# Kernel tuning notes

Hardware: AMD Instinct MI355X
Metric: run time of the kernel (lower is better)

## Reference

```python
import jax, jax.numpy as jnp
import numpy as np

B, S, D, H = 2, 2048, 1024, 16
DH = D // H  # dim_per_head = 64


def setup_inputs() -> dict:
    key = jax.random.key(0)
    ks = jax.random.split(key, 12)
    scale = 1.0 / np.sqrt(D)
    inp = {
        "key": jax.random.normal(ks[0], (B, S, D), jnp.float32),
        "value": jax.random.normal(ks[1], (B, S, D), jnp.float32),
        "query": jax.random.normal(ks[2], (B, S, D), jnp.float32),
        "mask": jax.random.randint(ks[3], (B, S, S), 0, 2) == 1,
        "Wq": jax.random.normal(ks[4], (D, D), jnp.float32) * scale,
        "bq": jnp.zeros((D,), jnp.float32),
        "Wk": jax.random.normal(ks[5], (D, D), jnp.float32) * scale,
        "bk": jnp.zeros((D,), jnp.float32),
        "Wv": jax.random.normal(ks[6], (D, D), jnp.float32) * scale,
        "bv": jnp.zeros((D,), jnp.float32),
        "Wo": jax.random.normal(ks[7], (D, D), jnp.float32) * scale,
        "bo": jnp.zeros((D,), jnp.float32),
    }
    return inp


def reference(key, value, query, mask, Wq, bq, Wk, bk, Wv, bv, Wo, bo):
    b, s, d = query.shape
    dh = d // H

    def split_heads(x):  # [b, s, d] -> [b, H, s, dh]
        return x.reshape(b, -1, H, dh).transpose(0, 2, 1, 3)

    q = split_heads(query @ Wq + bq) / jnp.sqrt(jnp.float32(dh))
    k = split_heads(key @ Wk + bk)
    v = split_heads(value @ Wv + bv)

    scores = jnp.einsum("bhqd,bhkd->bhqk", q, k)  # [b, H, s, s]
    scores = jnp.where(mask[:, None, :, :], jnp.float32(-1e18), scores)
    attn = jax.nn.softmax(scores, axis=-1)  # dropout is identity in eval
    ctx = jnp.einsum("bhqk,bhkd->bhqd", attn, v)
    ctx = ctx.transpose(0, 2, 1, 3).reshape(b, s, d)
    return ctx @ Wo + bo
```

## Files before the change

kernel.cpp:

```cpp
#include <hip/hip_runtime.h>
#include <hip/hip_bf16.h>

#define BATCH  2
#define SEQ    2048
#define DMODEL 1024
#define NHEAD  16
#define DHEAD  64
#define NTOK   (BATCH * SEQ)

using f32x4  = __attribute__((ext_vector_type(4))) float;
using f32x16 = __attribute__((ext_vector_type(16))) float;
using s16x4  = __attribute__((ext_vector_type(4))) short;
using s16x8  = __attribute__((ext_vector_type(8))) short;

__device__ __forceinline__ short f2bf(float f) {
  __hip_bfloat16 h = __float2bfloat16(f);
  return *(short*)&h;
}

__device__ __forceinline__ void gload_lds16(const short* g, short* l) {
  __builtin_amdgcn_global_load_lds(
      (const __attribute__((address_space(1))) void*)g,
      (__attribute__((address_space(3))) void*)l, 16, 0, 0);
}

__global__ __launch_bounds__(256) void wtrans_kernel(
    const float* __restrict__ Wq, const float* __restrict__ Wk,
    const float* __restrict__ Wv, const float* __restrict__ Wo,
    short* __restrict__ Wt) {
  __shared__ short tile[64][72];
  const float* W = blockIdx.z == 0 ? Wq : blockIdx.z == 1 ? Wk
                 : blockIdx.z == 2 ? Wv : Wo;
  short* out = Wt + (size_t)blockIdx.z * DMODEL * DMODEL;
  int k0 = blockIdx.x * 64, n0 = blockIdx.y * 64;
  int t = threadIdx.x;
#pragma unroll
  for (int i = 0; i < 4; ++i) {
    int idx = t + i * 256;
    int row = idx >> 4, c4 = idx & 15;
    f32x4 v = *(const f32x4*)(W + (size_t)(k0 + row) * DMODEL + n0 + c4 * 4);
    s16x4 p;
    p[0] = f2bf(v[0]); p[1] = f2bf(v[1]); p[2] = f2bf(v[2]); p[3] = f2bf(v[3]);
    *(s16x4*)&tile[row][c4 * 4] = p;
  }
  __syncthreads();
#pragma unroll
  for (int i = 0; i < 2; ++i) {
    int idx = t + i * 256;
    int nrow = idx >> 3, c8 = idx & 7;
    s16x8 p;
#pragma unroll
    for (int j = 0; j < 8; ++j) p[j] = tile[c8 * 8 + j][nrow];
    *(s16x8*)(out + (size_t)(n0 + nrow) * DMODEL + k0 + c8 * 8) = p;
  }
}

__global__ __launch_bounds__(256) void xcast_kernel(
    const float* __restrict__ Xq, const float* __restrict__ Xk,
    const float* __restrict__ Xv, short* __restrict__ Xb) {
  int sel = blockIdx.y;
  const float* src = sel == 0 ? Xq : sel == 1 ? Xk : Xv;
  size_t off = ((size_t)blockIdx.x * 256 + threadIdx.x) * 8;
  f32x4 v0 = *(const f32x4*)(src + off);
  f32x4 v1 = *(const f32x4*)(src + off + 4);
  s16x8 p;
  p[0] = f2bf(v0[0]); p[1] = f2bf(v0[1]); p[2] = f2bf(v0[2]); p[3] = f2bf(v0[3]);
  p[4] = f2bf(v1[0]); p[5] = f2bf(v1[1]); p[6] = f2bf(v1[2]); p[7] = f2bf(v1[3]);
  *(s16x8*)(Xb + (size_t)sel * NTOK * DMODEL + off) = p;
}

__global__ __launch_bounds__(256) void mpack_kernel(
    const int* __restrict__ mask, unsigned long long* __restrict__ Mp) {
  const int total_words = BATCH * SEQ * (SEQ / 64);
  int lane = threadIdx.x & 63;
  int wv = blockIdx.x * 4 + (threadIdx.x >> 6);
  int nw = gridDim.x * 4;
  for (int w = wv; w < total_words; w += nw) {
    int mv = mask[(size_t)w * 64 + lane];
    unsigned long long bits = __ballot(mv != 0);
    if (lane == 0) Mp[w] = bits;
  }
}

__global__ __launch_bounds__(256) void proj_qkv_kernel(
    const short* __restrict__ Xb, const short* __restrict__ Wt,
    const float* __restrict__ bq, const float* __restrict__ bk,
    const float* __restrict__ bv, short* __restrict__ QKV) {
  __shared__ short As[2][128 * 32];
  __shared__ short Bs[2][128 * 32];
  int wg = blockIdx.x;
  int orig = (wg & 7) * 96 + (wg >> 3);
  int sel = orig >> 8;
  int rem = orig & 255;
  int mx = rem >> 3, ny = rem & 7;

  const short* X    = Xb + (size_t)sel * NTOK * DMODEL;
  const float* bias = sel == 0 ? bq : sel == 1 ? bk : bv;
  const short* Wsel = Wt + (size_t)sel * DMODEL * DMODEL;
  short* Obuf = QKV + (size_t)sel * ((size_t)BATCH * NHEAD * SEQ * DHEAD);
  const float scale = sel == 0 ? 0.18033688011111793f : 1.0f;

  int m0 = mx * 128, n0 = ny * 128;
  int t = threadIdx.x, wid = t >> 6, lane = t & 63;
  int lr = lane & 15, lg = lane >> 4;
  int wr = wid >> 1, wc = wid & 1;
  f32x4 acc[4][4] = {};

  const int gr0 = t >> 2, gc0 = (t & 3) << 3;
  const short* Ax0 = X + (size_t)(m0 + gr0) * DMODEL + gc0;
  const short* Ax1 = Ax0 + (size_t)64 * DMODEL;
  const short* Bw0 = Wsel + (size_t)(n0 + gr0) * DMODEL + gc0;
  const short* Bw1 = Bw0 + (size_t)64 * DMODEL;
  const int lofs0 = (t & ~63) << 3, lofs1 = lofs0 + 256 * 8;

#define STAGEQ(bufi, k0s) {                                                   \
    gload_lds16(Ax0 + (k0s), &As[bufi][0] + lofs0);                           \
    gload_lds16(Ax1 + (k0s), &As[bufi][0] + lofs1);                           \
    gload_lds16(Bw0 + (k0s), &Bs[bufi][0] + lofs0);                           \
    gload_lds16(Bw1 + (k0s), &Bs[bufi][0] + lofs1); }

  STAGEQ(0, 0);
  __syncthreads();

  int cur = 0;
  for (int kt = 0; kt < DMODEL / 32; ++kt) {
    if (kt + 1 < DMODEL / 32) STAGEQ(cur ^ 1, (kt + 1) * 32);
    s16x8 afr[4], bfr[4];
#pragma unroll
    for (int mi = 0; mi < 4; ++mi)
      afr[mi] = *(const s16x8*)(&As[cur][0] + (wr * 64 + mi * 16 + lr) * 32 + lg * 8);
#pragma unroll
    for (int ni = 0; ni < 4; ++ni)
      bfr[ni] = *(const s16x8*)(&Bs[cur][0] + (wc * 64 + ni * 16 + lr) * 32 + lg * 8);
    __builtin_amdgcn_s_setprio(1);
#pragma unroll
    for (int mi = 0; mi < 4; ++mi)
#pragma unroll
      for (int ni = 0; ni < 4; ++ni)
        acc[mi][ni] = __builtin_amdgcn_mfma_f32_16x16x32_bf16(
            afr[mi], bfr[ni], acc[mi][ni], 0, 0, 0);
    __builtin_amdgcn_s_setprio(0);
    __syncthreads();
    cur ^= 1;
  }
#undef STAGEQ

  if (sel == 2) {
    int bq_ = m0 >> 11;
    int s0 = (m0 & (SEQ - 1)) + wr * 64 + lg * 4;
#pragma unroll
    for (int mi = 0; mi < 4; ++mi)
#pragma unroll
      for (int ni = 0; ni < 4; ++ni) {
        int n = n0 + wc * 64 + ni * 16 + lr;
        float bv_ = bias[n];
        int h = n >> 6, d = n & 63;
        s16x4 pk;
#pragma unroll
        for (int r = 0; r < 4; ++r) pk[r] = f2bf(acc[mi][ni][r] + bv_);
        *(s16x4*)&Obuf[((size_t)(bq_ * NHEAD + h) * DHEAD + d) * SEQ
                       + s0 + mi * 16] = pk;
      }
  } else {
#pragma unroll
    for (int mi = 0; mi < 4; ++mi)
#pragma unroll
      for (int ni = 0; ni < 4; ++ni) {
        int n = n0 + wc * 64 + ni * 16 + lr;
        float bv_ = bias[n];
        int h = n >> 6, d = n & 63;
#pragma unroll
        for (int r = 0; r < 4; ++r) {
          int m = m0 + wr * 64 + mi * 16 + lg * 4 + r;
          int b = m >> 11, s = m & (SEQ - 1);
          float val = (acc[mi][ni][r] + bv_) * scale;
          Obuf[((size_t)(b * NHEAD + h) * SEQ + s) * DHEAD + d] = f2bf(val);
        }
      }
  }
}

__global__ __launch_bounds__(256) void attn_kernel(
    const short* __restrict__ Qb, const short* __restrict__ Kb,
    const short* __restrict__ VbT, const unsigned long long* __restrict__ Mp,
    short* __restrict__ Ctx) {
  __shared__ short Ks[2][64 * 64];
  __shared__ short Vt[2][64 * 64];
  int wg = blockIdx.x;
  int orig = (wg & 7) * 64 + (wg >> 3);
  int bh = orig >> 4, qt = orig & 15;
  int b = bh >> 4, h = bh & 15;
  int q0 = qt * 128;
  int t = threadIdx.x, wid = t >> 6, lane = t & 63;
  int ql = lane & 31, hi = lane >> 5;
  int qrow = q0 + wid * 32 + ql;

  const short* Qp = Qb + ((size_t)bh * SEQ + qrow) * DHEAD + hi * 8;
  s16x8 qf[4];
#pragma unroll
  for (int ds = 0; ds < 4; ++ds) qf[ds] = *(const s16x8*)(Qp + ds * 16);

  const short* KbB = Kb + (size_t)bh * SEQ * DHEAD;
  const short* VtB = VbT + (size_t)bh * DHEAD * SEQ;

  const int srow = lane >> 3;
  const int schunk = ((lane & 7) ^ srow) * 8;

  int offK[4];
#pragma unroll
  for (int j = 0; j < 4; ++j)
    offK[j] = ql * 64 + (((j * 2 + hi) ^ (ql & 7)) << 3);
  int offVa[4], offVb[4];
#pragma unroll
  for (int m = 0; m < 4; ++m) {
    offVa[m] = ql * 64 + (((m * 2)     ^ (ql & 7)) << 3) + 4 * hi;
    offVb[m] = ql * 64 + (((m * 2 + 1) ^ (ql & 7)) << 3) + 4 * hi;
  }

  float m_run = -1e30f, l_run = 0.f;
  f32x16 oacc0 = {}, oacc1 = {};

  const unsigned long long* mrow = Mp + ((size_t)b * SEQ + qrow) * (SEQ / 64);

#define STAGE(bufi, k0s)                                                      \
  {                                                                           \
    _Pragma("unroll")                                                         \
    for (int i = 0; i < 2; ++i) {                                             \
      int rbase = wid * 16 + i * 8;                                           \
      gload_lds16(KbB + (size_t)((k0s) + rbase + srow) * DHEAD + schunk,      \
                  &Ks[bufi][rbase * 64]);                                     \
      gload_lds16(VtB + (size_t)(rbase + srow) * SEQ + (k0s) + schunk,        \
                  &Vt[bufi][rbase * 64]);                                     \
    }                                                                         \
  }

  unsigned long long mw_cur = mrow[0];
  STAGE(0, 0);
  asm volatile("s_waitcnt vmcnt(0)" ::: "memory");
  __syncthreads();

  int cur = 0;
  for (int kt = 0; kt < SEQ / 64; ++kt) {
    unsigned long long mw_next = 0;
    if (kt + 1 < SEQ / 64) {
      STAGE(cur ^ 1, (kt + 1) * 64);
      mw_next = mrow[kt + 1];
    }
    const short* KsC = Ks[cur];
    const short* VtC = Vt[cur];

    f32x16 sf0 = {}, sf1 = {};
    __builtin_amdgcn_s_setprio(1);
#pragma unroll
    for (int ds = 0; ds < 4; ++ds) {
      s16x8 k0 = *(const s16x8*)&KsC[offK[ds]];
      s16x8 k1 = *(const s16x8*)&KsC[offK[ds] + 2048];
      sf0 = __builtin_amdgcn_mfma_f32_32x32x16_bf16(k0, qf[ds], sf0, 0, 0, 0);
      sf1 = __builtin_amdgcn_mfma_f32_32x32x16_bf16(k1, qf[ds], sf1, 0, 0, 0);
    }
    __builtin_amdgcn_s_setprio(0);

    unsigned h0 = ((unsigned)mw_cur) >> (hi << 2);
    unsigned h1 = ((unsigned)(mw_cur >> 32)) >> (hi << 2);
#pragma unroll
    for (int r = 0; r < 16; ++r) {
      const int c = (r & 3) + 8 * (r >> 2);
      if ((h0 >> c) & 1u) sf0[r] = -1e30f;
      if ((h1 >> c) & 1u) sf1[r] = -1e30f;
    }

    float tm = sf0[0];
#pragma unroll
    for (int r = 1; r < 16; ++r) tm = fmaxf(tm, sf0[r]);
#pragma unroll
    for (int r = 0; r < 16; ++r) tm = fmaxf(tm, sf1[r]);
    tm = fmaxf(tm, __shfl_xor(tm, 32, 64));

    bool small = __all(tm <= m_run + 8.0f);
    if (!small) {
      float mnew = fmaxf(m_run, tm);
      float scl = __builtin_amdgcn_exp2f(m_run - mnew);
      m_run = mnew;
      l_run *= scl;
#pragma unroll
      for (int r = 0; r < 16; ++r) {
        float s_ = __shfl(scl, (r & 3) + 8 * (r >> 2) + 4 * hi, 64);
        oacc0[r] *= s_;
        oacc1[r] *= s_;
      }
    }

    float ss = 0.f;
#pragma unroll
    for (int r = 0; r < 16; ++r) {
      sf0[r] = __builtin_amdgcn_exp2f(sf0[r] - m_run);
      sf1[r] = __builtin_amdgcn_exp2f(sf1[r] - m_run);
      ss += sf0[r] + sf1[r];
    }
    l_run += ss + __shfl_xor(ss, 32, 64);

    __builtin_amdgcn_s_setprio(1);
#pragma unroll
    for (int m = 0; m < 4; ++m) {
      const int base = (m & 1) * 8;
      s16x8 pa;
#pragma unroll
      for (int e = 0; e < 8; ++e)
        pa[e] = f2bf(m < 2 ? sf0[base + e] : sf1[base + e]);
      union { s16x4 q[2]; s16x8 v; } v0, v1;
      v0.q[0] = *(const s16x4*)&VtC[offVa[m]];
      v0.q[1] = *(const s16x4*)&VtC[offVb[m]];
      v1.q[0] = *(const s16x4*)&VtC[offVa[m] + 2048];
      v1.q[1] = *(const s16x4*)&VtC[offVb[m] + 2048];
      oacc0 = __builtin_amdgcn_mfma_f32_32x32x16_bf16(pa, v0.v, oacc0, 0, 0, 0);
      oacc1 = __builtin_amdgcn_mfma_f32_32x32x16_bf16(pa, v1.v, oacc1, 0, 0, 0);
    }
    __builtin_amdgcn_s_setprio(0);

    asm volatile("s_waitcnt vmcnt(0)" ::: "memory");
    __syncthreads();
    cur ^= 1;
    mw_cur = mw_next;
  }
#undef STAGE

#pragma unroll
  for (int r = 0; r < 16; ++r) {
    int c = (r & 3) + 8 * (r >> 2) + 4 * hi;
    float linv = 1.0f / __shfl(l_run, c, 64);
    int q_ = q0 + wid * 32 + c;
    size_t base = ((size_t)b * SEQ + q_) * DMODEL + h * DHEAD + ql;
    Ctx[base] = f2bf(oacc0[r] * linv);
    Ctx[base + 32] = f2bf(oacc1[r] * linv);
  }
}

__global__ __launch_bounds__(256) void proj_out_kernel(
    const short* __restrict__ Ctx, const short* __restrict__ Wot,
    const float* __restrict__ bo, float* __restrict__ Out) {
  __shared__ short As[2][128 * 32];
  __shared__ short Bs[2][128 * 32];
  int wg = blockIdx.x;
  int orig = (wg & 7) * 32 + (wg >> 3);
  int mx = orig >> 3, ny = orig & 7;
  int m0 = mx * 128, n0 = ny * 128;
  int t = threadIdx.x, wid = t >> 6, lane = t & 63;
  int lr = lane & 15, lg = lane >> 4;
  int wr = wid >> 1, wc = wid & 1;
  f32x4 acc[4][4] = {};

  const int gr0 = t >> 2, gc0 = (t & 3) << 3;
  const short* Actx0 = Ctx + (size_t)(m0 + gr0) * DMODEL + gc0;
  const short* Actx1 = Actx0 + (size_t)64 * DMODEL;
  const short* Bwo0 = Wot + (size_t)(n0 + gr0) * DMODEL + gc0;
  const short* Bwo1 = Bwo0 + (size_t)64 * DMODEL;
  const int lofs0 = (t & ~63) << 3, lofs1 = lofs0 + 256 * 8;

#define STAGE_PO(bufi, k0s) {                                                 \
    gload_lds16(Actx0 + (k0s), &As[bufi][0] + lofs0);                         \
    gload_lds16(Actx1 + (k0s), &As[bufi][0] + lofs1);                         \
    gload_lds16(Bwo0 + (k0s), &Bs[bufi][0] + lofs0);                          \
    gload_lds16(Bwo1 + (k0s), &Bs[bufi][0] + lofs1); }

  STAGE_PO(0, 0);
  __syncthreads();

  int cur = 0;
  for (int kt = 0; kt < DMODEL / 32; ++kt) {
    if (kt + 1 < DMODEL / 32) STAGE_PO(cur ^ 1, (kt + 1) * 32);
    s16x8 afr[4], bfr[4];
#pragma unroll
    for (int mi = 0; mi < 4; ++mi)
      afr[mi] = *(const s16x8*)(&As[cur][0] + (wr * 64 + mi * 16 + lr) * 32 + lg * 8);
#pragma unroll
    for (int ni = 0; ni < 4; ++ni)
      bfr[ni] = *(const s16x8*)(&Bs[cur][0] + (wc * 64 + ni * 16 + lr) * 32 + lg * 8);
    __builtin_amdgcn_s_setprio(1);
#pragma unroll
    for (int mi = 0; mi < 4; ++mi)
#pragma unroll
      for (int ni = 0; ni < 4; ++ni)
        acc[mi][ni] = __builtin_amdgcn_mfma_f32_16x16x32_bf16(
            afr[mi], bfr[ni], acc[mi][ni], 0, 0, 0);
    __builtin_amdgcn_s_setprio(0);
    __syncthreads();
    cur ^= 1;
  }
#undef STAGE_PO

#pragma unroll
  for (int mi = 0; mi < 4; ++mi)
#pragma unroll
    for (int ni = 0; ni < 4; ++ni) {
      int n = n0 + wc * 64 + ni * 16 + lr;
      float bv_ = bo[n];
#pragma unroll
      for (int r = 0; r < 4; ++r) {
        int m = m0 + wr * 64 + mi * 16 + lg * 4 + r;
        Out[(size_t)m * DMODEL + n] = acc[mi][ni][r] + bv_;
      }
    }
}

extern "C" void kernel_launch(void* const* d_in, const int* in_sizes, int n_in,
                              void* d_out, int out_size, void* d_ws, size_t ws_size,
                              hipStream_t stream) {
  const float* key_in   = (const float*)d_in[0];
  const float* value_in = (const float*)d_in[1];
  const float* query_in = (const float*)d_in[2];
  const int*   mask     = (const int*)d_in[3];
  const float* Wq = (const float*)d_in[4];
  const float* bq = (const float*)d_in[5];
  const float* Wk = (const float*)d_in[6];
  const float* bk = (const float*)d_in[7];
  const float* Wv = (const float*)d_in[8];
  const float* bv = (const float*)d_in[9];
  const float* Wo = (const float*)d_in[10];
  const float* bo = (const float*)d_in[11];
  float* out = (float*)d_out;

  short* ws = (short*)d_ws;
  const size_t WSZ   = (size_t)DMODEL * DMODEL;
  const size_t QKVSZ = (size_t)BATCH * NHEAD * SEQ * DHEAD;
  short* Wt  = ws;
  short* QKV = ws + 4 * WSZ;
  short* Qb  = QKV;
  short* Kb  = QKV + QKVSZ;
  short* VbT = QKV + 2 * QKVSZ;
  short* Xb  = ws + 4 * WSZ + 3 * QKVSZ;
  short* Ctx = Xb;
  unsigned long long* Mp = (unsigned long long*)ws;

  wtrans_kernel<<<dim3(16, 16, 4), 256, 0, stream>>>(Wq, Wk, Wv, Wo, Wt);
  xcast_kernel<<<dim3(2048, 3), 256, 0, stream>>>(query_in, key_in, value_in, Xb);
  proj_qkv_kernel<<<dim3(768), 256, 0, stream>>>(Xb, Wt, bq, bk, bv, QKV);
  mpack_kernel<<<dim3(1024), 256, 0, stream>>>(mask, Mp);
  attn_kernel<<<dim3(512), 256, 0, stream>>>(Qb, Kb, VbT, Mp, Ctx);
  proj_out_kernel<<<dim3(256), 256, 0, stream>>>(Ctx, Wt + 3 * WSZ, bo, out);
}
```

Measured before the change: 183.9 us.

## Merge prep kernels and triple-buffer LDS pipelines in GEMMs and attention

Fuses the weight transpose, input cast and mask packing into one prep kernel and moves the packed mask buffer into the output buffer, so the mask packing no longer has to wait for the QKV projection. Switches the QKV projection, attention and output projection loops from double to triple-buffered LDS staging, using partial vmcnt waits and one barrier per iteration to hide load latency. In attention it also defers the cross-half max and sum shuffles, doing the sum once at the end. Raises LDS use per block, which may lower occupancy, and relies on the output buffer being overwritten only after attention has read the mask.

```diff
diff --git a/kernel.cpp b/kernel.cpp
--- a/kernel.cpp
+++ b/kernel.cpp
@@ -24,61 +24,58 @@
       (__attribute__((address_space(3))) void*)l, 16, 0, 0);
 }
 
-__global__ __launch_bounds__(256) void wtrans_kernel(
+__global__ __launch_bounds__(256) void prep_kernel(
     const float* __restrict__ Wq, const float* __restrict__ Wk,
     const float* __restrict__ Wv, const float* __restrict__ Wo,
-    short* __restrict__ Wt) {
+    short* __restrict__ Wt,
+    const float* __restrict__ Xq, const float* __restrict__ Xk,
+    const float* __restrict__ Xv, short* __restrict__ Xb,
+    const int* __restrict__ mask, unsigned long long* __restrict__ Mp) {
   __shared__ short tile[64][72];
-  const float* W = blockIdx.z == 0 ? Wq : blockIdx.z == 1 ? Wk
-                 : blockIdx.z == 2 ? Wv : Wo;
-  short* out = Wt + (size_t)blockIdx.z * DMODEL * DMODEL;
-  int k0 = blockIdx.x * 64, n0 = blockIdx.y * 64;
-  int t = threadIdx.x;
-#pragma unroll
-  for (int i = 0; i < 4; ++i) {
-    int idx = t + i * 256;
-    int row = idx >> 4, c4 = idx & 15;
-    f32x4 v = *(const f32x4*)(W + (size_t)(k0 + row) * DMODEL + n0 + c4 * 4);
-    s16x4 p;
-    p[0] = f2bf(v[0]); p[1] = f2bf(v[1]); p[2] = f2bf(v[2]); p[3] = f2bf(v[3]);
-    *(s16x4*)&tile[row][c4 * 4] = p;
-  }
-  __syncthreads();
-#pragma unroll
-  for (int i = 0; i < 2; ++i) {
-    int idx = t + i * 256;
-    int nrow = idx >> 3, c8 = idx & 7;
+  int bid = blockIdx.x, t = threadIdx.x;
+  if (bid < 1024) {
+    int z = bid >> 8, rem = bid & 255, x = rem & 15, y = rem >> 4;
+    const float* W = z == 0 ? Wq : z == 1 ? Wk : z == 2 ? Wv : Wo;
+    short* out = Wt + (size_t)z * DMODEL * DMODEL;
+    int k0 = x * 64, n0 = y * 64;
+#pragma unroll
+    for (int i = 0; i < 4; ++i) {
+      int idx = t + i * 256, row = idx >> 4, c4 = idx & 15;
+      f32x4 v = *(const f32x4*)(W + (size_t)(k0 + row) * DMODEL + n0 + c4 * 4);
+      s16x4 p;
+      p[0] = f2bf(v[0]); p[1] = f2bf(v[1]); p[2] = f2bf(v[2]); p[3] = f2bf(v[3]);
+      *(s16x4*)&tile[row][c4 * 4] = p;
+    }
+    __syncthreads();
+#pragma unroll
+    for (int i = 0; i < 2; ++i) {
+      int idx = t + i * 256, nrow = idx >> 3, c8 = idx & 7;
+      s16x8 p;
+#pragma unroll
+      for (int j = 0; j < 8; ++j) p[j] = tile[c8 * 8 + j][nrow];
+      *(s16x8*)(out + (size_t)(n0 + nrow) * DMODEL + k0 + c8 * 8) = p;
+    }
+  } else if (bid < 7168) {
+    int r = bid - 1024;
+    int sel = r >> 11, bx = r & 2047;
+    const float* src = sel == 0 ? Xq : sel == 1 ? Xk : Xv;
+    size_t off = ((size_t)bx * 256 + t) * 8;
+    f32x4 v0 = *(const f32x4*)(src + off);
+    f32x4 v1 = *(const f32x4*)(src + off + 4);
     s16x8 p;
-#pragma unroll
-    for (int j = 0; j < 8; ++j) p[j] = tile[c8 * 8 + j][nrow];
-    *(s16x8*)(out + (size_t)(n0 + nrow) * DMODEL + k0 + c8 * 8) = p;
-  }
-}
-
-__global__ __launch_bounds__(256) void xcast_kernel(
-    const float* __restrict__ Xq, const float* __restrict__ Xk,
-    const float* __restrict__ Xv, short* __restrict__ Xb) {
-  int sel = blockIdx.y;
-  const float* src = sel == 0 ? Xq : sel == 1 ? Xk : Xv;
-  size_t off = ((size_t)blockIdx.x * 256 + threadIdx.x) * 8;
-  f32x4 v0 = *(const f32x4*)(src + off);
-  f32x4 v1 = *(const f32x4*)(src + off + 4);
-  s16x8 p;
-  p[0] = f2bf(v0[0]); p[1] = f2bf(v0[1]); p[2] = f2bf(v0[2]); p[3] = f2bf(v0[3]);
-  p[4] = f2bf(v1[0]); p[5] = f2bf(v1[1]); p[6] = f2bf(v1[2]); p[7] = f2bf(v1[3]);
-  *(s16x8*)(Xb + (size_t)sel * NTOK * DMODEL + off) = p;
-}
-
-__global__ __launch_bounds__(256) void mpack_kernel(
-    const int* __restrict__ mask, unsigned long long* __restrict__ Mp) {
-  const int total_words = BATCH * SEQ * (SEQ / 64);
-  int lane = threadIdx.x & 63;
-  int wv = blockIdx.x * 4 + (threadIdx.x >> 6);
-  int nw = gridDim.x * 4;
-  for (int w = wv; w < total_words; w += nw) {
-    int mv = mask[(size_t)w * 64 + lane];
-    unsigned long long bits = __ballot(mv != 0);
-    if (lane == 0) Mp[w] = bits;
+    p[0] = f2bf(v0[0]); p[1] = f2bf(v0[1]); p[2] = f2bf(v0[2]); p[3] = f2bf(v0[3]);
+    p[4] = f2bf(v1[0]); p[5] = f2bf(v1[1]); p[6] = f2bf(v1[2]); p[7] = f2bf(v1[3]);
+    *(s16x8*)(Xb + (size_t)sel * NTOK * DMODEL + off) = p;
+  } else {
+    int bx = bid - 7168;
+    const int total_words = BATCH * SEQ * (SEQ / 64);
+    int lane = t & 63;
+    int wv = bx * 4 + (t >> 6);
+    for (int w = wv; w < total_words; w += 4096) {
+      int mv = mask[(size_t)w * 64 + lane];
+      unsigned long long bits = __ballot(mv != 0);
+      if (lane == 0) Mp[w] = bits;
+    }
   }
 }
 
@@ -86,8 +83,8 @@
     const short* __restrict__ Xb, const short* __restrict__ Wt,
     const float* __restrict__ bq, const float* __restrict__ bk,
     const float* __restrict__ bv, short* __restrict__ QKV) {
-  __shared__ short As[2][128 * 32];
-  __shared__ short Bs[2][128 * 32];
+  __shared__ short As[3][128 * 32];
+  __shared__ short Bs[3][128 * 32];
   int wg = blockIdx.x;
   int orig = (wg & 7) * 96 + (wg >> 3);
   int sel = orig >> 8;
@@ -120,18 +117,25 @@
     gload_lds16(Bw1 + (k0s), &Bs[bufi][0] + lofs1); }
 
   STAGEQ(0, 0);
-  __syncthreads();
-
-  int cur = 0;
-  for (int kt = 0; kt < DMODEL / 32; ++kt) {
-    if (kt + 1 < DMODEL / 32) STAGEQ(cur ^ 1, (kt + 1) * 32);
+  STAGEQ(1, 32);
+
+  int cb = 0;
+  for (int kt = 0; kt < 32; ++kt) {
+    if (kt + 1 < 32) { asm volatile("s_waitcnt vmcnt(4)" ::: "memory"); }
+    else             { asm volatile("s_waitcnt vmcnt(0)" ::: "memory"); }
+    __builtin_amdgcn_sched_barrier(0);
+    __builtin_amdgcn_s_barrier();
+    __builtin_amdgcn_sched_barrier(0);
+    int st = cb + 2; if (st > 2) st -= 3;
+    if (kt + 2 < 32) STAGEQ(st, (kt + 2) * 32);
+
     s16x8 afr[4], bfr[4];
 #pragma unroll
     for (int mi = 0; mi < 4; ++mi)
-      afr[mi] = *(const s16x8*)(&As[cur][0] + (wr * 64 + mi * 16 + lr) * 32 + lg * 8);
+      afr[mi] = *(const s16x8*)(&As[cb][0] + (wr * 64 + mi * 16 + lr) * 32 + lg * 8);
 #pragma unroll
     for (int ni = 0; ni < 4; ++ni)
-      bfr[ni] = *(const s16x8*)(&Bs[cur][0] + (wc * 64 + ni * 16 + lr) * 32 + lg * 8);
+      bfr[ni] = *(const s16x8*)(&Bs[cb][0] + (wc * 64 + ni * 16 + lr) * 32 + lg * 8);
     __builtin_amdgcn_s_setprio(1);
 #pragma unroll
     for (int mi = 0; mi < 4; ++mi)
@@ -140,8 +144,7 @@
         acc[mi][ni] = __builtin_amdgcn_mfma_f32_16x16x32_bf16(
             afr[mi], bfr[ni], acc[mi][ni], 0, 0, 0);
     __builtin_amdgcn_s_setprio(0);
-    __syncthreads();
-    cur ^= 1;
+    cb = (cb == 2) ? 0 : cb + 1;
   }
 #undef STAGEQ
 
@@ -184,8 +187,8 @@
     const short* __restrict__ Qb, const short* __restrict__ Kb,
     const short* __restrict__ VbT, const unsigned long long* __restrict__ Mp,
     short* __restrict__ Ctx) {
-  __shared__ short Ks[2][64 * 64];
-  __shared__ short Vt[2][64 * 64];
+  __shared__ short Ks[3][64 * 64];
+  __shared__ short Vt[3][64 * 64];
   int wg = blockIdx.x;
   int orig = (wg & 7) * 64 + (wg >> 3);
   int bh = orig >> 4, qt = orig & 15;
@@ -234,20 +237,25 @@
     }                                                                         \
   }
 
-  unsigned long long mw_cur = mrow[0];
+  unsigned long long mwq0 = mrow[0], mwq1 = mrow[1];
   STAGE(0, 0);
-  asm volatile("s_waitcnt vmcnt(0)" ::: "memory");
-  __syncthreads();
-
-  int cur = 0;
-  for (int kt = 0; kt < SEQ / 64; ++kt) {
-    unsigned long long mw_next = 0;
-    if (kt + 1 < SEQ / 64) {
-      STAGE(cur ^ 1, (kt + 1) * 64);
-      mw_next = mrow[kt + 1];
-    }
-    const short* KsC = Ks[cur];
-    const short* VtC = Vt[cur];
+  STAGE(1, 64);
+
+  int cb = 0;
+  for (int kt = 0; kt < 32; ++kt) {
+    if (kt + 1 < 32) { asm volatile("s_waitcnt vmcnt(4)" ::: "memory"); }
+    else             { asm volatile("s_waitcnt vmcnt(0)" ::: "memory"); }
+    __builtin_amdgcn_sched_barrier(0);
+    __builtin_amdgcn_s_barrier();
+    __builtin_amdgcn_sched_barrier(0);
+    int st = cb + 2; if (st > 2) st -= 3;
+    if (kt + 2 < 32) STAGE(st, (kt + 2) * 64);
+    unsigned long long mw_cur = mwq0;
+    mwq0 = mwq1;
+    if (kt + 2 < 32) mwq1 = mrow[kt + 2];
+
+    const short* KsC = Ks[cb];
+    const short* VtC = Vt[cb];
 
     f32x16 sf0 = {}, sf1 = {};
     __builtin_amdgcn_s_setprio(1);
@@ -274,11 +282,11 @@
     for (int r = 1; r < 16; ++r) tm = fmaxf(tm, sf0[r]);
 #pragma unroll
     for (int r = 0; r < 16; ++r) tm = fmaxf(tm, sf1[r]);
-    tm = fmaxf(tm, __shfl_xor(tm, 32, 64));
 
     bool small = __all(tm <= m_run + 8.0f);
     if (!small) {
-      float mnew = fmaxf(m_run, tm);
+      float tmx = fmaxf(tm, __shfl_xor(tm, 32, 64));
+      float mnew = fmaxf(m_run, tmx);
       float scl = __builtin_amdgcn_exp2f(m_run - mnew);
       m_run = mnew;
       l_run *= scl;
@@ -297,7 +305,7 @@
       sf1[r] = __builtin_amdgcn_exp2f(sf1[r] - m_run);
       ss += sf0[r] + sf1[r];
     }
-    l_run += ss + __shfl_xor(ss, 32, 64);
+    l_run += ss;
 
     __builtin_amdgcn_s_setprio(1);
 #pragma unroll
@@ -316,18 +324,15 @@
       oacc1 = __builtin_amdgcn_mfma_f32_32x32x16_bf16(pa, v1.v, oacc1, 0, 0, 0);
     }
     __builtin_amdgcn_s_setprio(0);
-
-    asm volatile("s_waitcnt vmcnt(0)" ::: "memory");
-    __syncthreads();
-    cur ^= 1;
-    mw_cur = mw_next;
+    cb = (cb == 2) ? 0 : cb + 1;
   }
 #undef STAGE
 
+  float l_tot = l_run + __shfl_xor(l_run, 32, 64);
 #pragma unroll
   for (int r = 0; r < 16; ++r) {
     int c = (r & 3) + 8 * (r >> 2) + 4 * hi;
-    float linv = 1.0f / __shfl(l_run, c, 64);
+    float linv = 1.0f / __shfl(l_tot, c, 64);
     int q_ = q0 + wid * 32 + c;
     size_t base = ((size_t)b * SEQ + q_) * DMODEL + h * DHEAD + ql;
     Ctx[base] = f2bf(oacc0[r] * linv);
@@ -338,8 +343,8 @@
 __global__ __launch_bounds__(256) void proj_out_kernel(
     const short* __restrict__ Ctx, const short* __restrict__ Wot,
     const float* __restrict__ bo, float* __restrict__ Out) {
-  __shared__ short As[2][128 * 32];
-  __shared__ short Bs[2][128 * 32];
+  __shared__ short As[3][128 * 32];
+  __shared__ short Bs[3][128 * 32];
   int wg = blockIdx.x;
   int orig = (wg & 7) * 32 + (wg >> 3);
   int mx = orig >> 3, ny = orig & 7;
@@ -363,18 +368,25 @@
     gload_lds16(Bwo1 + (k0s), &Bs[bufi][0] + lofs1); }
 
   STAGE_PO(0, 0);
-  __syncthreads();
-
-  int cur = 0;
-  for (int kt = 0; kt < DMODEL / 32; ++kt) {
-    if (kt + 1 < DMODEL / 32) STAGE_PO(cur ^ 1, (kt + 1) * 32);
+  STAGE_PO(1, 32);
+
+  int cb = 0;
+  for (int kt = 0; kt < 32; ++kt) {
+    if (kt + 1 < 32) { asm volatile("s_waitcnt vmcnt(4)" ::: "memory"); }
+    else             { asm volatile("s_waitcnt vmcnt(0)" ::: "memory"); }
+    __builtin_amdgcn_sched_barrier(0);
+    __builtin_amdgcn_s_barrier();
+    __builtin_amdgcn_sched_barrier(0);
+    int st = cb + 2; if (st > 2) st -= 3;
+    if (kt + 2 < 32) STAGE_PO(st, (kt + 2) * 32);
+
     s16x8 afr[4], bfr[4];
 #pragma unroll
     for (int mi = 0; mi < 4; ++mi)
-      afr[mi] = *(const s16x8*)(&As[cur][0] + (wr * 64 + mi * 16 + lr) * 32 + lg * 8);
+      afr[mi] = *(const s16x8*)(&As[cb][0] + (wr * 64 + mi * 16 + lr) * 32 + lg * 8);
 #pragma unroll
     for (int ni = 0; ni < 4; ++ni)
-      bfr[ni] = *(const s16x8*)(&Bs[cur][0] + (wc * 64 + ni * 16 + lr) * 32 + lg * 8);
+      bfr[ni] = *(const s16x8*)(&Bs[cb][0] + (wc * 64 + ni * 16 + lr) * 32 + lg * 8);
     __builtin_amdgcn_s_setprio(1);
 #pragma unroll
     for (int mi = 0; mi < 4; ++mi)
@@ -383,8 +395,7 @@
         acc[mi][ni] = __builtin_amdgcn_mfma_f32_16x16x32_bf16(
             afr[mi], bfr[ni], acc[mi][ni], 0, 0, 0);
     __builtin_amdgcn_s_setprio(0);
-    __syncthreads();
-    cur ^= 1;
+    cb = (cb == 2) ? 0 : cb + 1;
   }
 #undef STAGE_PO
 
@@ -429,12 +440,11 @@
   short* VbT = QKV + 2 * QKVSZ;
   short* Xb  = ws + 4 * WSZ + 3 * QKVSZ;
   short* Ctx = Xb;
-  unsigned long long* Mp = (unsigned long long*)ws;
-
-  wtrans_kernel<<<dim3(16, 16, 4), 256, 0, stream>>>(Wq, Wk, Wv, Wo, Wt);
-  xcast_kernel<<<dim3(2048, 3), 256, 0, stream>>>(query_in, key_in, value_in, Xb);
+  unsigned long long* Mp = (unsigned long long*)d_out;
+
+  prep_kernel<<<dim3(8192), 256, 0, stream>>>(
+      Wq, Wk, Wv, Wo, Wt, query_in, key_in, value_in, Xb, mask, Mp);
   proj_qkv_kernel<<<dim3(768), 256, 0, stream>>>(Xb, Wt, bq, bk, bv, QKV);
-  mpack_kernel<<<dim3(1024), 256, 0, stream>>>(mask, Mp);
   attn_kernel<<<dim3(512), 256, 0, stream>>>(Qb, Kb, VbT, Mp, Ctx);
   proj_out_kernel<<<dim3(256), 256, 0, stream>>>(Ctx, Wt + 3 * WSZ, bo, out);
 }
```

After: 168.2 us. 8.6% less time.
